# Optimization experiments

Measured on AMD Instinct MI355X. Metric: run time of the kernel, lower is better.

The kernel has to match this reference:

```python
import jax, jax.numpy as jnp
import numpy as np

TEMPERATURE = 0.07
EPS = 1e-12  # matches torch F.normalize default eps


def setup_inputs() -> dict:
    key = jax.random.key(0)
    k1, k2 = jax.random.split(key)
    N, D = 8192, 1024
    return {
        "query": jax.random.normal(k1, (N, D), dtype=jnp.float32),
        "key": jax.random.normal(k2, (N, D), dtype=jnp.float32),
    }


def _l2_normalize(x):
    norm = jnp.sqrt(jnp.sum(x * x, axis=-1, keepdims=True))
    return x / jnp.maximum(norm, EPS)


def reference(query, key):
    q = _l2_normalize(query)            # [N, D]
    k = _l2_normalize(key)              # [N, D]
    logits = jnp.einsum("nd,md->nm", q, k) / TEMPERATURE  # [N, N]
    # cross-entropy with diagonal labels = mean(logsumexp(row) - diag)
    diag = jnp.diagonal(logits)
    fwd_loss = jnp.mean(jax.nn.logsumexp(logits, axis=1) - diag)
    bwd_loss = jnp.mean(jax.nn.logsumexp(logits, axis=0) - diag)
    return 0.5 * (fwd_loss + bwd_loss)
```

## Files before the change

### kernel.cpp

```cpp
#include <hip/hip_runtime.h>
#include <math.h>

#define N 8192
#define D 1024
#define INV_T 14.285714285714286f

typedef unsigned short ushortT;
typedef unsigned int uintT;
typedef __bf16 bf16x8 __attribute__((ext_vector_type(8)));
typedef float f32x4 __attribute__((ext_vector_type(4)));

#define AS1 __attribute__((address_space(1)))
#define AS3 __attribute__((address_space(3)))

__device__ __forceinline__ ushortT f2bf(float x) {
    uintT u = __float_as_uint(x);
    return (ushortT)((u + 0x7fffu + ((u >> 16) & 1u)) >> 16);
}

__global__ __launch_bounds__(256)
void normalize_bf16_kernel(const float* __restrict__ q, const float* __restrict__ k,
                           ushortT* __restrict__ qh, ushortT* __restrict__ kh,
                           float* __restrict__ diag,
                           float* __restrict__ rowsum, float* __restrict__ colsum,
                           float* __restrict__ out) {
    const int wid  = threadIdx.x >> 6;
    const int lane = threadIdx.x & 63;
    const int row  = blockIdx.x * 4 + wid;
    if (lane == 60) rowsum[row] = 0.f;
    if (lane == 61) colsum[row] = 0.f;
    if (row == 0 && lane == 62) out[0] = INV_T;

    const float* qr = q + (size_t)row * D;
    const float* kr = k + (size_t)row * D;
    float4 a[4], b[4];
    #pragma unroll
    for (int j = 0; j < 4; ++j) {
        a[j] = *(const float4*)(qr + j * 256 + lane * 4);
        b[j] = *(const float4*)(kr + j * 256 + lane * 4);
    }
    float sqq = 0.f, skk = 0.f, sqk = 0.f;
    #pragma unroll
    for (int j = 0; j < 4; ++j) {
        sqq += a[j].x*a[j].x + a[j].y*a[j].y + a[j].z*a[j].z + a[j].w*a[j].w;
        skk += b[j].x*b[j].x + b[j].y*b[j].y + b[j].z*b[j].z + b[j].w*b[j].w;
        sqk += a[j].x*b[j].x + a[j].y*b[j].y + a[j].z*b[j].z + a[j].w*b[j].w;
    }
    #pragma unroll
    for (int m = 1; m < 64; m <<= 1) {
        sqq += __shfl_xor(sqq, m, 64);
        skk += __shfl_xor(skk, m, 64);
        sqk += __shfl_xor(sqk, m, 64);
    }
    const float iq = 1.0f / fmaxf(sqrtf(sqq), 1e-12f);
    const float ik = 1.0f / fmaxf(sqrtf(skk), 1e-12f);
    if (lane == 0) diag[row] = sqk * iq * ik * INV_T;

    #pragma unroll
    for (int j = 0; j < 4; ++j) {
        float av[4] = {a[j].x * iq, a[j].y * iq, a[j].z * iq, a[j].w * iq};
        float bv[4] = {b[j].x * ik, b[j].y * ik, b[j].z * ik, b[j].w * ik};
        ushort4 qv, kv;
        ushortT* qp = (ushortT*)&qv; ushortT* kp = (ushortT*)&kv;
        #pragma unroll
        for (int e = 0; e < 4; ++e) { qp[e] = f2bf(av[e]); kp[e] = f2bf(bv[e]); }
        *(ushort4*)(qh + (size_t)row * D + j * 256 + lane * 4) = qv;
        *(ushort4*)(kh + (size_t)row * D + j * 256 + lane * 4) = kv;
    }
}

#define LBUF 65536
#define NT 16

__global__ __launch_bounds__(512, 2)
void mfma256_lse_kernel(const ushortT* __restrict__ qh, const ushortT* __restrict__ kh,
                        float* __restrict__ rowsum, float* __restrict__ colsum) {
    __shared__ __align__(16) char lds[2 * LBUF];

    const int wg  = blockIdx.x;
    const int swz = (wg & 7) * 128 + (wg >> 3);
    const int bi  = swz >> 5;
    const int bj  = swz & 31;

    const int tid  = threadIdx.x;
    const int w    = tid >> 6;
    const int lane = tid & 63;
    const int wm   = w >> 2, wn = w & 3;
    const int la   = lane & 15, lq = lane >> 4;

    size_t aoff[4], boff[4];
    int dstb[4];
    #pragma unroll
    for (int i = 0; i < 4; ++i) {
        int lin = i * 512 + tid;
        int r   = lin >> 3;
        int s   = lin & 7;
        int sp  = s ^ (r & 7);
        aoff[i] = (size_t)(bi * 256 + r) * D + sp * 8;
        boff[i] = (size_t)(bj * 256 + r) * D + sp * 8;
        dstb[i] = lin * 16;
    }

    int byteA[8][2], byteB[4][2];
    #pragma unroll
    for (int f = 0; f < 8; ++f) {
        int ra = wm * 128 + f * 16 + la;
        byteA[f][0] = ra * 128 + ((lq       ^ (ra & 7)) * 16);
        byteA[f][1] = ra * 128 + (((lq ^ 4) ^ (ra & 7)) * 16);
    }
    #pragma unroll
    for (int n = 0; n < 4; ++n) {
        int rb = wn * 64 + n * 16 + la;
        byteB[n][0] = 32768 + rb * 128 + ((lq       ^ (rb & 7)) * 16);
        byteB[n][1] = 32768 + rb * 128 + (((lq ^ 4) ^ (rb & 7)) * 16);
    }

    f32x4 acc[8][4] = {};

#define STAGE(t1) do { \
    char* db_ = lds + (((t1) & 1) * LBUF); \
    const size_t kof_ = (size_t)(t1) * 64; \
    _Pragma("unroll") \
    for (int i_ = 0; i_ < 4; ++i_) { \
        __builtin_amdgcn_global_load_lds( \
            (const AS1 void*)(qh + aoff[i_] + kof_), \
            (AS3 void*)(db_ + dstb[i_]), 16, 0, 0); \
        __builtin_amdgcn_global_load_lds( \
            (const AS1 void*)(kh + boff[i_] + kof_), \
            (AS3 void*)(db_ + 32768 + dstb[i_]), 16, 0, 0); \
    } } while (0)

#define BAR() __builtin_amdgcn_s_barrier()

    STAGE(0);
    asm volatile("s_waitcnt vmcnt(0)" ::: "memory");
    BAR();

    #pragma unroll 1
    for (int t = 0; t < NT; ++t) {
        const char* bufb = lds + (t & 1) * LBUF;

        if (t < NT - 1) STAGE(t + 1);

        bf16x8 bk[4], aF[4];

        #pragma unroll
        for (int n = 0; n < 4; ++n) bk[n] = *(const bf16x8*)(bufb + byteB[n][0]);
        #pragma unroll
        for (int f = 0; f < 4; ++f) aF[f] = *(const bf16x8*)(bufb + byteA[f][0]);
        BAR();
        __builtin_amdgcn_s_setprio(1);
        #pragma unroll
        for (int f = 0; f < 4; ++f)
            #pragma unroll
            for (int n = 0; n < 4; ++n)
                acc[f][n] = __builtin_amdgcn_mfma_f32_16x16x32_bf16(aF[f], bk[n], acc[f][n], 0, 0, 0);
        __builtin_amdgcn_s_setprio(0);
        BAR();

        #pragma unroll
        for (int f = 0; f < 4; ++f) aF[f] = *(const bf16x8*)(bufb + byteA[f + 4][0]);
        BAR();
        __builtin_amdgcn_s_setprio(1);
        #pragma unroll
        for (int f = 0; f < 4; ++f)
            #pragma unroll
            for (int n = 0; n < 4; ++n)
                acc[f + 4][n] = __builtin_amdgcn_mfma_f32_16x16x32_bf16(aF[f], bk[n], acc[f + 4][n], 0, 0, 0);
        __builtin_amdgcn_s_setprio(0);
        BAR();

        #pragma unroll
        for (int n = 0; n < 4; ++n) bk[n] = *(const bf16x8*)(bufb + byteB[n][1]);
        #pragma unroll
        for (int f = 0; f < 4; ++f) aF[f] = *(const bf16x8*)(bufb + byteA[f][1]);
        BAR();
        __builtin_amdgcn_s_setprio(1);
        #pragma unroll
        for (int f = 0; f < 4; ++f)
            #pragma unroll
            for (int n = 0; n < 4; ++n)
                acc[f][n] = __builtin_amdgcn_mfma_f32_16x16x32_bf16(aF[f], bk[n], acc[f][n], 0, 0, 0);
        __builtin_amdgcn_s_setprio(0);
        BAR();

        #pragma unroll
        for (int f = 0; f < 4; ++f) aF[f] = *(const bf16x8*)(bufb + byteA[f + 4][1]);
        BAR();
        __builtin_amdgcn_s_setprio(1);
        #pragma unroll
        for (int f = 0; f < 4; ++f)
            #pragma unroll
            for (int n = 0; n < 4; ++n)
                acc[f + 4][n] = __builtin_amdgcn_mfma_f32_16x16x32_bf16(aF[f], bk[n], acc[f + 4][n], 0, 0, 0);
        __builtin_amdgcn_s_setprio(0);
        asm volatile("s_waitcnt vmcnt(0)" ::: "memory");
        BAR();
    }
#undef STAGE
#undef BAR

    #pragma unroll
    for (int f = 0; f < 8; ++f)
        #pragma unroll
        for (int n = 0; n < 4; ++n)
            #pragma unroll
            for (int r = 0; r < 4; ++r)
                acc[f][n][r] = __expf((acc[f][n][r] - 1.0f) * INV_T);

    #pragma unroll
    for (int f = 0; f < 8; ++f)
        #pragma unroll
        for (int r = 0; r < 4; ++r) {
            float v = acc[f][0][r] + acc[f][1][r] + acc[f][2][r] + acc[f][3][r];
            v += __shfl_xor(v, 1, 64);
            v += __shfl_xor(v, 2, 64);
            v += __shfl_xor(v, 4, 64);
            v += __shfl_xor(v, 8, 64);
            if (la == 0)
                atomicAdd(&rowsum[bi * 256 + wm * 128 + f * 16 + lq * 4 + r], v);
        }

    #pragma unroll
    for (int n = 0; n < 4; ++n) {
        float v = 0.f;
        #pragma unroll
        for (int f = 0; f < 8; ++f)
            #pragma unroll
            for (int r = 0; r < 4; ++r)
                v += acc[f][n][r];
        v += __shfl_xor(v, 16, 64);
        v += __shfl_xor(v, 32, 64);
        if (lq == 0)
            atomicAdd(&colsum[bj * 256 + wn * 64 + n * 16 + la], v);
    }
}

__global__ __launch_bounds__(1024)
void final_kernel(const float* __restrict__ rowsum, const float* __restrict__ colsum,
                  const float* __restrict__ diag, float* __restrict__ out) {
    const int tid = threadIdx.x;
    const int i = blockIdx.x * 1024 + tid;
    float p = 0.5f * (logf(rowsum[i]) + logf(colsum[i])) - diag[i];
    #pragma unroll
    for (int m = 1; m < 64; m <<= 1) p += __shfl_xor(p, m, 64);
    __shared__ float red[16];
    const int wid = tid >> 6, lane = tid & 63;
    if (lane == 0) red[wid] = p;
    __syncthreads();
    if (tid == 0) {
        float t = 0.f;
        #pragma unroll
        for (int w = 0; w < 16; ++w) t += red[w];
        atomicAdd(out, t / (float)N);
    }
}

#define BT 128
__global__ __launch_bounds__(256)
void norms_diag_kernel(const float* __restrict__ q, const float* __restrict__ k,
                       float* __restrict__ invq, float* __restrict__ invk,
                       float* __restrict__ diag, float* __restrict__ out) {
    const int row = blockIdx.x;
    const int tid = threadIdx.x;
    if (row == 0 && tid == 66) out[0] = INV_T;
    float4 a = *(const float4*)(q + (size_t)row * D + tid * 4);
    float4 b = *(const float4*)(k + (size_t)row * D + tid * 4);
    float sqq = a.x*a.x + a.y*a.y + a.z*a.z + a.w*a.w;
    float skk = b.x*b.x + b.y*b.y + b.z*b.z + b.w*b.w;
    float sqk = a.x*b.x + a.y*b.y + a.z*b.z + a.w*b.w;
    #pragma unroll
    for (int m = 1; m < 64; m <<= 1) {
        sqq += __shfl_xor(sqq, m, 64);
        skk += __shfl_xor(skk, m, 64);
        sqk += __shfl_xor(sqk, m, 64);
    }
    __shared__ float red[3][4];
    const int wid = tid >> 6, lane = tid & 63;
    if (lane == 0) { red[0][wid] = sqq; red[1][wid] = skk; red[2][wid] = sqk; }
    __syncthreads();
    if (tid == 0) {
        float s0 = red[0][0] + red[0][1] + red[0][2] + red[0][3];
        float s1 = red[1][0] + red[1][1] + red[1][2] + red[1][3];
        float s2 = red[2][0] + red[2][1] + red[2][2] + red[2][3];
        float iq = 1.0f / fmaxf(sqrtf(s0), 1e-12f);
        float ik = 1.0f / fmaxf(sqrtf(s1), 1e-12f);
        invq[row] = iq; invk[row] = ik;
        diag[row] = s2 * iq * ik * INV_T;
    }
}

#define KBF 16
#define LDTF 132
__global__ __launch_bounds__(256)
void gemm_lse_kernel(const float* __restrict__ q, const float* __restrict__ k,
                     const float* __restrict__ invq, const float* __restrict__ invk,
                     float* __restrict__ rowsum, float* __restrict__ colsum) {
    __shared__ float As[KBF * LDTF];
    __shared__ float Bs[KBF * LDTF];
    const int tid = threadIdx.x;
    const int tx = tid & 15;
    const int ty = tid >> 4;
    const int bi = blockIdx.y;
    const int bj = blockIdx.x;
    const float* qb = q + (size_t)(bi * BT) * D;
    const float* kb = k + (size_t)(bj * BT) * D;
    float acc[8][8] = {};
    for (int k0 = 0; k0 < D; k0 += KBF) {
        #pragma unroll
        for (int i = 0; i < 2; ++i) {
            int idx  = tid + i * 256;
            int row  = idx >> 2;
            int kc4  = idx & 3;
            float4 av = *(const float4*)(qb + (size_t)row * D + k0 + kc4 * 4);
            float4 bv = *(const float4*)(kb + (size_t)row * D + k0 + kc4 * 4);
            int base = (kc4 * 4) * LDTF + row;
            As[base] = av.x; As[base + LDTF] = av.y; As[base + 2*LDTF] = av.z; As[base + 3*LDTF] = av.w;
            Bs[base] = bv.x; Bs[base + LDTF] = bv.y; Bs[base + 2*LDTF] = bv.z; Bs[base + 3*LDTF] = bv.w;
        }
        __syncthreads();
        #pragma unroll
        for (int kk = 0; kk < KBF; ++kk) {
            const float* ap = &As[kk * LDTF + ty * 8];
            const float* bp = &Bs[kk * LDTF + tx * 8];
            float4 a0 = *(const float4*)(ap);
            float4 a1 = *(const float4*)(ap + 4);
            float4 b0 = *(const float4*)(bp);
            float4 b1 = *(const float4*)(bp + 4);
            float ar[8] = {a0.x, a0.y, a0.z, a0.w, a1.x, a1.y, a1.z, a1.w};
            float br[8] = {b0.x, b0.y, b0.z, b0.w, b1.x, b1.y, b1.z, b1.w};
            #pragma unroll
            for (int r = 0; r < 8; ++r)
                #pragma unroll
                for (int c = 0; c < 8; ++c)
                    acc[r][c] += ar[r] * br[c];
        }
        __syncthreads();
    }
    float iqr[8], ikc[8];
    #pragma unroll
    for (int r = 0; r < 8; ++r) iqr[r] = invq[bi * BT + ty * 8 + r] * INV_T;
    #pragma unroll
    for (int c = 0; c < 8; ++c) ikc[c] = invk[bj * BT + tx * 8 + c];
    float rowpart[8] = {};
    float colpart[8] = {};
    #pragma unroll
    for (int r = 0; r < 8; ++r)
        #pragma unroll
        for (int c = 0; c < 8; ++c) {
            float e = __expf(acc[r][c] * iqr[r] * ikc[c] - INV_T);
            rowpart[r] += e; colpart[c] += e;
        }
    #pragma unroll
    for (int r = 0; r < 8; ++r) {
        float v = rowpart[r];
        v += __shfl_xor(v, 1, 64); v += __shfl_xor(v, 2, 64);
        v += __shfl_xor(v, 4, 64); v += __shfl_xor(v, 8, 64);
        if (tx == 0) atomicAdd(&rowsum[bi * BT + ty * 8 + r], v);
    }
    __syncthreads();
    float* colbuf = As;
    #pragma unroll
    for (int c = 0; c < 8; ++c) colbuf[ty * 128 + tx * 8 + c] = colpart[c];
    __syncthreads();
    if (tid < 128) {
        float s = 0.f;
        #pragma unroll
        for (int t2 = 0; t2 < 16; ++t2) s += colbuf[t2 * 128 + tid];
        atomicAdd(&colsum[bj * BT + tid], s);
    }
}

extern "C" void kernel_launch(void* const* d_in, const int* in_sizes, int n_in,
                              void* d_out, int out_size, void* d_ws, size_t ws_size,
                              hipStream_t stream) {
    const float* q = (const float*)d_in[0];
    const float* k = (const float*)d_in[1];

    const size_t planeBytes = 2ull * N * D * sizeof(ushortT);
    const size_t needFast   = planeBytes + 3ull * N * sizeof(float);

    if (ws_size >= needFast) {
        ushortT* qh = (ushortT*)d_ws;
        ushortT* kh = qh + (size_t)N * D;
        float* tail  = (float*)((char*)d_ws + planeBytes);
        float* rowsum = tail;
        float* colsum = tail + N;
        float* diag   = tail + 2 * N;

        normalize_bf16_kernel<<<N / 4, 256, 0, stream>>>(q, k, qh, kh, diag,
                                                         rowsum, colsum, (float*)d_out);
        mfma256_lse_kernel<<<(N / 256) * (N / 256), 512, 0, stream>>>(qh, kh, rowsum, colsum);
        final_kernel<<<N / 1024, 1024, 0, stream>>>(rowsum, colsum, diag, (float*)d_out);
    } else {
        float* ws     = (float*)d_ws;
        float* invq   = ws;
        float* invk   = ws + N;
        float* rowsum = ws + 2 * N;
        float* colsum = ws + 3 * N;
        float* diag   = ws + 4 * N;
        hipMemsetAsync(rowsum, 0, 2ull * N * sizeof(float), stream);
        norms_diag_kernel<<<N, 256, 0, stream>>>(q, k, invq, invk, diag, (float*)d_out);
        gemm_lse_kernel<<<dim3(N / BT, N / BT), 256, 0, stream>>>(q, k, invq, invk, rowsum, colsum);
        final_kernel<<<N / 1024, 1024, 0, stream>>>(rowsum, colsum, diag, (float*)d_out);
    }
}
```

Baseline: 297.7 us.

## Interleave next-tile global loads across MFMA phases and remap warp fragments

The next K-tile prefetch is split into four quarter-stages, each issued between the MFMA phases with partial vmcnt waits and explicit lgkmcnt waits, replacing one bulk prefetch at loop start followed by a full drain at loop end. Each wave's A and B fragments are also remapped to interleaved halves of the tile rather than contiguous blocks, with the atomic index math updated to match. The aim is to spread memory traffic more evenly across the compute phases and to change the LDS access pattern, at the cost of more fragile wait-count ordering.

```diff
diff --git a/kernel.cpp b/kernel.cpp
--- a/kernel.cpp
+++ b/kernel.cpp
@@ -73,8 +73,8 @@
 #define NT 16
 
 __global__ __launch_bounds__(512, 2)
-void mfma256_lse_kernel(const ushortT* __restrict__ qh, const ushortT* __restrict__ kh,
-                        float* __restrict__ rowsum, float* __restrict__ colsum) {
+void mfma8p_lse_kernel(const ushortT* __restrict__ qh, const ushortT* __restrict__ kh,
+                       float* __restrict__ rowsum, float* __restrict__ colsum) {
     __shared__ __align__(16) char lds[2 * LBUF];
 
     const int wg  = blockIdx.x;
@@ -104,51 +104,48 @@
     int byteA[8][2], byteB[4][2];
     #pragma unroll
     for (int f = 0; f < 8; ++f) {
-        int ra = wm * 128 + f * 16 + la;
+        int ra = ((f >= 4) ? 128 : 0) + wm * 64 + (f & 3) * 16 + la;
         byteA[f][0] = ra * 128 + ((lq       ^ (ra & 7)) * 16);
         byteA[f][1] = ra * 128 + (((lq ^ 4) ^ (ra & 7)) * 16);
     }
     #pragma unroll
     for (int n = 0; n < 4; ++n) {
-        int rb = wn * 64 + n * 16 + la;
+        int rb = ((n >= 2) ? 128 : 0) + wn * 32 + (n & 1) * 16 + la;
         byteB[n][0] = 32768 + rb * 128 + ((lq       ^ (rb & 7)) * 16);
         byteB[n][1] = 32768 + rb * 128 + (((lq ^ 4) ^ (rb & 7)) * 16);
     }
 
     f32x4 acc[8][4] = {};
 
-#define STAGE(t1) do { \
-    char* db_ = lds + (((t1) & 1) * LBUF); \
-    const size_t kof_ = (size_t)(t1) * 64; \
-    _Pragma("unroll") \
-    for (int i_ = 0; i_ < 4; ++i_) { \
-        __builtin_amdgcn_global_load_lds( \
-            (const AS1 void*)(qh + aoff[i_] + kof_), \
-            (AS3 void*)(db_ + dstb[i_]), 16, 0, 0); \
-        __builtin_amdgcn_global_load_lds( \
-            (const AS1 void*)(kh + boff[i_] + kof_), \
-            (AS3 void*)(db_ + 32768 + dstb[i_]), 16, 0, 0); \
-    } } while (0)
-
-#define BAR() __builtin_amdgcn_s_barrier()
-
-    STAGE(0);
-    asm volatile("s_waitcnt vmcnt(0)" ::: "memory");
+#define GLD(srcp, dstp) __builtin_amdgcn_global_load_lds((const AS1 void*)(srcp), (AS3 void*)(dstp), 16, 0, 0)
+#define STAGE_A(h, t1) do { char* db_ = lds + (((t1) & 1) * LBUF); \
+    GLD(qh + aoff[(h)*2]     + (size_t)(t1) * 64, db_ + dstb[(h)*2]); \
+    GLD(qh + aoff[(h)*2 + 1] + (size_t)(t1) * 64, db_ + dstb[(h)*2 + 1]); } while (0)
+#define STAGE_B(h, t1) do { char* db_ = lds + (((t1) & 1) * LBUF); \
+    GLD(kh + boff[(h)*2]     + (size_t)(t1) * 64, db_ + 32768 + dstb[(h)*2]); \
+    GLD(kh + boff[(h)*2 + 1] + (size_t)(t1) * 64, db_ + 32768 + dstb[(h)*2 + 1]); } while (0)
+
+#define BAR()   __builtin_amdgcn_s_barrier()
+#define LGKM0() asm volatile("s_waitcnt lgkmcnt(0)" ::: "memory")
+#define VM2()   asm volatile("s_waitcnt vmcnt(2)" ::: "memory")
+#define VM0()   asm volatile("s_waitcnt vmcnt(0)" ::: "memory")
+
+    STAGE_B(0, 0); STAGE_B(1, 0); STAGE_A(0, 0); STAGE_A(1, 0);
+    VM0();
     BAR();
 
     #pragma unroll 1
     for (int t = 0; t < NT; ++t) {
         const char* bufb = lds + (t & 1) * LBUF;
-
-        if (t < NT - 1) STAGE(t + 1);
-
-        bf16x8 bk[4], aF[4];
+        const bool last = (t == NT - 1);
+        bf16x8 aF[4], bk[4];
 
         #pragma unroll
         for (int n = 0; n < 4; ++n) bk[n] = *(const bf16x8*)(bufb + byteB[n][0]);
         #pragma unroll
         for (int f = 0; f < 4; ++f) aF[f] = *(const bf16x8*)(bufb + byteA[f][0]);
-        BAR();
+        if (!last) { STAGE_B(0, t + 1); VM2(); } else { VM0(); }
+        BAR(); LGKM0();
         __builtin_amdgcn_s_setprio(1);
         #pragma unroll
         for (int f = 0; f < 4; ++f)
@@ -160,7 +157,8 @@
 
         #pragma unroll
         for (int f = 0; f < 4; ++f) aF[f] = *(const bf16x8*)(bufb + byteA[f + 4][0]);
-        BAR();
+        if (!last) STAGE_B(1, t + 1);
+        BAR(); LGKM0();
         __builtin_amdgcn_s_setprio(1);
         #pragma unroll
         for (int f = 0; f < 4; ++f)
@@ -174,7 +172,8 @@
         for (int n = 0; n < 4; ++n) bk[n] = *(const bf16x8*)(bufb + byteB[n][1]);
         #pragma unroll
         for (int f = 0; f < 4; ++f) aF[f] = *(const bf16x8*)(bufb + byteA[f][1]);
-        BAR();
+        if (!last) STAGE_A(0, t + 1);
+        BAR(); LGKM0();
         __builtin_amdgcn_s_setprio(1);
         #pragma unroll
         for (int f = 0; f < 4; ++f)
@@ -186,7 +185,8 @@
 
         #pragma unroll
         for (int f = 0; f < 4; ++f) aF[f] = *(const bf16x8*)(bufb + byteA[f + 4][1]);
-        BAR();
+        if (!last) { STAGE_A(1, t + 1); VM2(); }
+        BAR(); LGKM0();
         __builtin_amdgcn_s_setprio(1);
         #pragma unroll
         for (int f = 0; f < 4; ++f)
@@ -194,11 +194,15 @@
             for (int n = 0; n < 4; ++n)
                 acc[f + 4][n] = __builtin_amdgcn_mfma_f32_16x16x32_bf16(aF[f], bk[n], acc[f + 4][n], 0, 0, 0);
         __builtin_amdgcn_s_setprio(0);
-        asm volatile("s_waitcnt vmcnt(0)" ::: "memory");
         BAR();
     }
-#undef STAGE
+#undef GLD
+#undef STAGE_A
+#undef STAGE_B
 #undef BAR
+#undef LGKM0
+#undef VM2
+#undef VM0
 
     #pragma unroll
     for (int f = 0; f < 8; ++f)
@@ -218,7 +222,7 @@
             v += __shfl_xor(v, 4, 64);
             v += __shfl_xor(v, 8, 64);
             if (la == 0)
-                atomicAdd(&rowsum[bi * 256 + wm * 128 + f * 16 + lq * 4 + r], v);
+                atomicAdd(&rowsum[bi * 256 + ((f >= 4) ? 128 : 0) + wm * 64 + (f & 3) * 16 + lq * 4 + r], v);
         }
 
     #pragma unroll
@@ -232,7 +236,7 @@
         v += __shfl_xor(v, 16, 64);
         v += __shfl_xor(v, 32, 64);
         if (lq == 0)
-            atomicAdd(&colsum[bj * 256 + wn * 64 + n * 16 + la], v);
+            atomicAdd(&colsum[bj * 256 + ((n >= 2) ? 128 : 0) + wn * 32 + (n & 1) * 16 + la], v);
     }
 }
 
@@ -390,7 +394,7 @@
 
         normalize_bf16_kernel<<<N / 4, 256, 0, stream>>>(q, k, qh, kh, diag,
                                                          rowsum, colsum, (float*)d_out);
-        mfma256_lse_kernel<<<(N / 256) * (N / 256), 512, 0, stream>>>(qh, kh, rowsum, colsum);
+        mfma8p_lse_kernel<<<(N / 256) * (N / 256), 512, 0, stream>>>(qh, kh, rowsum, colsum);
         final_kernel<<<N / 1024, 1024, 0, stream>>>(rowsum, colsum, diag, (float*)d_out);
     } else {
         float* ws     = (float*)d_ws;
```

Result: slower. 379.8 us (+27.6%).
